# Kernel optimization log

Hardware: AMD Instinct MI355X
Metric: run time of the kernel (lower is better)

The kernel has to match this reference:

```python
import jax, jax.numpy as jnp
import numpy as np

H = 8  # num_heads

def setup_inputs() -> dict:
    key = jax.random.key(0)
    ks = jax.random.split(key, 8)
    N, B, E = 1024, 8, 256
    value = jax.random.normal(ks[0], (N, B, E), dtype=jnp.float32)
    pos = jax.random.normal(ks[1], (B * H, N, N), dtype=jnp.float32)
    s = 1.0 / np.sqrt(E)
    in_proj_w = jax.random.uniform(ks[2], (3 * E, E), jnp.float32, -s, s)   # content attn qkv proj
    in_proj_b = jnp.zeros((3 * E,), jnp.float32)
    out_w = jax.random.uniform(ks[3], (E, E), jnp.float32, -s, s)
    out_b = jnp.zeros((E,), jnp.float32)
    return {"value": value, "position_attention_weights": pos,
            "in_proj_w": in_proj_w, "in_proj_b": in_proj_b,
            "out_w": out_w, "out_b": out_b}

def reference(value, position_attention_weights, in_proj_w, in_proj_b, out_w, out_b):
    # value: (N, B, E) seq-first, position_attention_weights: (B*H, N, N)
    N, B, E = value.shape
    Dh = E // H
    qkv = value @ in_proj_w.T + in_proj_b            # (N, B, 3E)
    q, k, v = jnp.split(qkv, 3, axis=-1)
    # (N, B, E) -> (B*H, N, Dh)
    def to_heads(t):
        return t.reshape(N, B * H, Dh).transpose(1, 0, 2)
    q, k, v = to_heads(q), to_heads(k), to_heads(v)
    scale = 1.0 / jnp.sqrt(jnp.asarray(Dh, q.dtype))
    content = jnp.einsum('bnd,bmd->bnm', q * scale, k)   # (B*H, N, N) content scores
    # merge_attention == 'gate': clamp both, log-sigmoid gate on positional, add
    content = jnp.clip(content, -10.0, 10.0)
    pos = jnp.clip(position_attention_weights, -10.0, 10.0)
    scores = jax.nn.log_sigmoid(pos) + content
    attn = jax.nn.softmax(scores, axis=-1)               # normalizer
    out = jnp.einsum('bnm,bmd->bnd', attn, v)            # (B*H, N, Dh)
    out = out.transpose(1, 0, 2).reshape(N, B, E)        # back to (N, B, E)
    out = out @ out_w.T + out_b
    attn_avg = attn.reshape(B, H, N, N).mean(axis=1)     # averaged attention weights
    return out, attn_avg
```

## Files before the change

kernel.cpp:

```cpp
#include <hip/hip_runtime.h>
#include <hip/hip_bf16.h>

typedef __attribute__((ext_vector_type(8))) short short8;
typedef __attribute__((ext_vector_type(4))) float f32x4;
typedef __attribute__((ext_vector_type(4))) unsigned short u16x4;

#define MFMA16(a,b,c) __builtin_amdgcn_mfma_f32_16x16x32_bf16((a),(b),(c),0,0,0)

__device__ __forceinline__ ushort f2bf(float x) {
  union { float f; unsigned u; } v; v.f = x;
  unsigned u = v.u;
  u = (u + 0x7fffu + ((u >> 16) & 1u)) >> 16;
  return (ushort)u;
}

__device__ __forceinline__ float bf2f(ushort u) {
  union { unsigned u; float f; } v; v.u = ((unsigned)u) << 16;
  return v.f;
}

__device__ __forceinline__ short8 ld8(const ushort* p) {
  return *reinterpret_cast<const short8*>(p);
}

__device__ __forceinline__ f32x4 ld4(const float* p) {
  return *reinterpret_cast<const f32x4*>(p);
}

__global__ void conv_kernel(const float* __restrict__ value,
                            const float* __restrict__ w_in,
                            const float* __restrict__ w_out,
                            ushort* __restrict__ vbf,
                            ushort* __restrict__ wbf,
                            ushort* __restrict__ owbf) {
  int i = blockIdx.x * 256 + threadIdx.x;
  const float* src; ushort* dst; int j;
  if (i < 524288)      { src = value; dst = vbf;  j = i; }
  else if (i < 573440) { src = w_in;  dst = wbf;  j = i - 524288; }
  else                 { src = w_out; dst = owbf; j = i - 573440; }
  float4 v = reinterpret_cast<const float4*>(src)[j];
  u16x4 o;
  o[0] = f2bf(v.x); o[1] = f2bf(v.y); o[2] = f2bf(v.z); o[3] = f2bf(v.w);
  reinterpret_cast<u16x4*>(dst)[j] = o;
}

__global__ __launch_bounds__(256) void qkv_kernel(
    const ushort* __restrict__ vbf, const ushort* __restrict__ wbf,
    const float* __restrict__ bias,
    ushort* __restrict__ qh, ushort* __restrict__ kh, ushort* __restrict__ vv) {
  int tid = threadIdx.x;
  int wave = tid >> 6, lane = tid & 63;
  int lq = lane & 15, lg = lane >> 4;
  int r0 = blockIdx.x * 16;
  int c0 = (blockIdx.y * 4 + wave) * 16;
  f32x4 acc = {0.f, 0.f, 0.f, 0.f};
  const ushort* ap = vbf + (size_t)(r0 + lq) * 256 + lg * 8;
  const ushort* bp = wbf + (size_t)(c0 + lq) * 256 + lg * 8;
#pragma unroll
  for (int k0 = 0; k0 < 256; k0 += 32)
    acc = MFMA16(ld8(ap + k0), ld8(bp + k0), acc);
  int c = c0 + lq;
  float bv = bias[c];
#pragma unroll
  for (int r = 0; r < 4; ++r) {
    int row = r0 + lg * 4 + r;
    int n = row >> 3, b = row & 7;
    float v = acc[r] + bv;
    if (c < 256) {
      int h = c >> 5, d = c & 31;
      qh[((size_t)(b * 8 + h) * 1024 + n) * 32 + d] = f2bf(v * 0.17677669529663689f);
    } else if (c < 512) {
      int cc = c - 256, h = cc >> 5, d = cc & 31;
      kh[((size_t)(b * 8 + h) * 1024 + n) * 32 + d] = f2bf(v);
    } else {
      int cc = c - 512, h = cc >> 5, d = cc & 31;
      vv[((size_t)(b * 8 + h) * 1024 + n) * 32 + d] = f2bf(v);
    }
  }
}

__global__ __launch_bounds__(256) void vtrans_kernel(const ushort* __restrict__ vv,
                                                     ushort* __restrict__ vt) {
  __shared__ ushort t[32][73];
  int tid = threadIdx.x;
  int bh = blockIdx.y, m0 = blockIdx.x * 64;
  int mm = tid >> 2, d0 = (tid & 3) * 8;
  short8 v = ld8(vv + ((size_t)bh * 1024 + m0 + mm) * 32 + d0);
#pragma unroll
  for (int j = 0; j < 8; ++j) t[d0 + j][mm] = (ushort)v[j];
  __syncthreads();
  int d = tid >> 3, mg = (tid & 7) * 8;
  short8 o;
#pragma unroll
  for (int j = 0; j < 8; ++j) o[j] = (short)t[d][mg + j];
  *reinterpret_cast<short8*>(vt + ((size_t)bh * 32 + d) * 1024 + m0 + mg) = o;
}

__global__ __launch_bounds__(256, 2) void attn_kernel(
    const ushort* __restrict__ qh, const ushort* __restrict__ kh,
    const ushort* __restrict__ vt, const float* __restrict__ pos,
    ushort* __restrict__ ao, float* __restrict__ avg_out) {
  __shared__ float pvred[2][4][16][32];
  __shared__ float rowsumT[2][16][4];

  int tid = threadIdx.x;
  int wave = tid >> 6, lane = tid & 63;
  int lq = lane & 15, lg = lane >> 4;
  int b = blockIdx.x;
  int n0 = blockIdx.y * 16;
  int wbase = wave * 256;
  int ra = ((lq >> 2) << 3) + (lq & 3);

  float avg[8][8];
#pragma unroll
  for (int u = 0; u < 8; ++u)
#pragma unroll
    for (int i = 0; i < 8; ++i) avg[u][i] = 0.f;

  const float* pbase = pos + ((size_t)(b * 8) << 20) + (size_t)(n0 + lq) * 1024 + wbase + lg * 8;

  f32x4 pfa[2], pfb[2];
  pfa[0] = ld4(pbase);       pfb[0] = ld4(pbase + 4);
  pfa[1] = ld4(pbase + 32);  pfb[1] = ld4(pbase + 36);

  for (int h = 0; h < 8; ++h) {
    int bh = b * 8 + h;
    const ushort* kp = kh + (size_t)bh * 32768;
    const ushort* vp = vt + (size_t)bh * 32768;
    short8 qa = ld8(qh + ((size_t)bh * 1024 + n0 + lq) * 32 + lg * 8);

    f32x4 acc0 = {0.f, 0.f, 0.f, 0.f}, acc1 = {0.f, 0.f, 0.f, 0.f};
    float rs = 0.f;
    short8 wh[8];

#pragma unroll
    for (int u = 0; u < 8; ++u) {
      int mu = wbase + u * 32;
      f32x4 p0 = pfa[u & 1];
      f32x4 p1 = pfb[u & 1];
      short8 ka = ld8(kp + (size_t)(mu + ra) * 32 + lg * 8);
      short8 kb = ld8(kp + (size_t)(mu + ra + 4) * 32 + lg * 8);
      short8 va = ld8(vp + (size_t)lq * 1024 + mu + lg * 8);
      short8 vb = ld8(vp + (size_t)(lq + 16) * 1024 + mu + lg * 8);
      {
        int g = h * 8 + u + 2;
        int gc = g < 63 ? g : 63;
        const float* np = pbase + ((size_t)(gc >> 3) << 20) + (gc & 7) * 32;
        pfa[u & 1] = ld4(np);
        pfb[u & 1] = ld4(np + 4);
      }
      f32x4 z = {0.f, 0.f, 0.f, 0.f};
      f32x4 SA = MFMA16(ka, qa, z);
      f32x4 SB = MFMA16(kb, qa, z);
      short8 w8;
#pragma unroll
      for (int i = 0; i < 4; ++i) {
        float p = fminf(10.f, fmaxf(-10.f, p0[i]));
        float c = fminf(10.f, fmaxf(-10.f, SA[i]));
        float w = __expf(c - 10.f) * __builtin_amdgcn_rcpf(1.f + __expf(-p));
        rs += w;
        w8[i] = (short)f2bf(w);
      }
#pragma unroll
      for (int i = 0; i < 4; ++i) {
        float p = fminf(10.f, fmaxf(-10.f, p1[i]));
        float c = fminf(10.f, fmaxf(-10.f, SB[i]));
        float w = __expf(c - 10.f) * __builtin_amdgcn_rcpf(1.f + __expf(-p));
        rs += w;
        w8[4 + i] = (short)f2bf(w);
      }
      wh[u] = w8;
      acc0 = MFMA16(w8, va, acc0);
      acc1 = MFMA16(w8, vb, acc1);
    }
    rs += __shfl_xor(rs, 16);
    rs += __shfl_xor(rs, 32);
    int buf = h & 1;
    if (lane < 16) rowsumT[buf][lq][wave] = rs;
#pragma unroll
    for (int j = 0; j < 4; ++j) {
      pvred[buf][wave][lg * 4 + j][lq] = acc0[j];
      pvred[buf][wave][lg * 4 + j][lq + 16] = acc1[j];
    }
    __syncthreads();
    {
      float invr = __builtin_amdgcn_rcpf(rowsumT[buf][lq][0] + rowsumT[buf][lq][1] +
                                         rowsumT[buf][lq][2] + rowsumT[buf][lq][3]);
#pragma unroll
      for (int u = 0; u < 8; ++u)
#pragma unroll
        for (int i = 0; i < 8; ++i)
          avg[u][i] += bf2f((ushort)wh[u][i]) * invr;
      int n = tid >> 4, d = tid & 15;
      float invn = __builtin_amdgcn_rcpf(rowsumT[buf][n][0] + rowsumT[buf][n][1] +
                                         rowsumT[buf][n][2] + rowsumT[buf][n][3]);
      float s0 = pvred[buf][0][n][d] + pvred[buf][1][n][d] +
                 pvred[buf][2][n][d] + pvred[buf][3][n][d];
      float s1 = pvred[buf][0][n][d + 16] + pvred[buf][1][n][d + 16] +
                 pvred[buf][2][n][d + 16] + pvred[buf][3][n][d + 16];
      size_t base = ((size_t)(n0 + n) * 8 + b) * 256 + h * 32;
      ao[base + d] = f2bf(s0 * invn);
      ao[base + d + 16] = f2bf(s1 * invn);
    }
  }
  float* op = avg_out + (size_t)b * 1048576 + (size_t)(n0 + lq) * 1024 + wbase;
#pragma unroll
  for (int u = 0; u < 8; ++u) {
    f32x4 v0 = {avg[u][0] * 0.125f, avg[u][1] * 0.125f, avg[u][2] * 0.125f, avg[u][3] * 0.125f};
    f32x4 v1 = {avg[u][4] * 0.125f, avg[u][5] * 0.125f, avg[u][6] * 0.125f, avg[u][7] * 0.125f};
    __builtin_nontemporal_store(v0, reinterpret_cast<f32x4*>(op + u * 32 + lg * 8));
    __builtin_nontemporal_store(v1, reinterpret_cast<f32x4*>(op + u * 32 + lg * 8 + 4));
  }
}

__global__ __launch_bounds__(256) void oproj_kernel(
    const ushort* __restrict__ ao, const ushort* __restrict__ owbf,
    const float* __restrict__ ob, float* __restrict__ outp) {
  int tid = threadIdx.x;
  int wave = tid >> 6, lane = tid & 63;
  int lq = lane & 15, lg = lane >> 4;
  int r0 = blockIdx.x * 16;
  int c0 = (blockIdx.y * 4 + wave) * 16;
  f32x4 acc = {0.f, 0.f, 0.f, 0.f};
  const ushort* ap = ao + (size_t)(r0 + lq) * 256 + lg * 8;
  const ushort* bp = owbf + (size_t)(c0 + lq) * 256 + lg * 8;
#pragma unroll
  for (int k0 = 0; k0 < 256; k0 += 32)
    acc = MFMA16(ld8(ap + k0), ld8(bp + k0), acc);
  int c = c0 + lq;
  float bv = ob[c];
#pragma unroll
  for (int r = 0; r < 4; ++r) {
    int row = r0 + lg * 4 + r;
    outp[(size_t)row * 256 + c] = acc[r] + bv;
  }
}

extern "C" void kernel_launch(void* const* d_in, const int* in_sizes, int n_in,
                              void* d_out, int out_size, void* d_ws, size_t ws_size,
                              hipStream_t stream) {
  const float* value = (const float*)d_in[0];
  const float* pos   = (const float*)d_in[1];
  const float* w_in  = (const float*)d_in[2];
  const float* b_in  = (const float*)d_in[3];
  const float* w_out = (const float*)d_in[4];
  const float* b_out = (const float*)d_in[5];

  char* ws = (char*)d_ws;
  ushort* vbf  = (ushort*)(ws);
  ushort* wbf  = (ushort*)(ws + 4194304);
  ushort* owbf = (ushort*)(ws + 4587520);
  ushort* qh   = (ushort*)(ws + 4718592);
  ushort* kh   = (ushort*)(ws + 8912896);
  ushort* vv   = (ushort*)(ws + 13107200);
  ushort* vt   = (ushort*)(ws);
  ushort* ao   = (ushort*)(ws + 17301504);

  float* outp = (float*)d_out;
  float* avgp = outp + 2097152;

  conv_kernel<<<2304, 256, 0, stream>>>(value, w_in, w_out, vbf, wbf, owbf);
  qkv_kernel<<<dim3(512, 12), 256, 0, stream>>>(vbf, wbf, b_in, qh, kh, vv);
  vtrans_kernel<<<dim3(16, 64), 256, 0, stream>>>(vv, vt);
  attn_kernel<<<dim3(8, 64), 256, 0, stream>>>(qh, kh, vt, pos, ao, avgp);
  oproj_kernel<<<dim3(512, 4), 256, 0, stream>>>(ao, owbf, b_out, outp);
}
```

Before: 192.2 us.

## Split fused attention into score kernel and PV/average kernel via workspace

```diff
diff --git a/kernel.cpp b/kernel.cpp
--- a/kernel.cpp
+++ b/kernel.cpp
@@ -96,59 +96,33 @@
   *reinterpret_cast<short8*>(vt + ((size_t)bh * 32 + d) * 1024 + m0 + mg) = o;
 }
 
-__global__ __launch_bounds__(256, 2) void attn_kernel(
+__global__ __launch_bounds__(256, 4) void score_kernel(
     const ushort* __restrict__ qh, const ushort* __restrict__ kh,
-    const ushort* __restrict__ vt, const float* __restrict__ pos,
-    ushort* __restrict__ ao, float* __restrict__ avg_out) {
-  __shared__ float pvred[2][4][16][32];
-  __shared__ float rowsumT[2][16][4];
-
+    const float* __restrict__ pos, ushort* __restrict__ wbuf,
+    float* __restrict__ rsum) {
   int tid = threadIdx.x;
   int wave = tid >> 6, lane = tid & 63;
   int lq = lane & 15, lg = lane >> 4;
   int b = blockIdx.x;
   int n0 = blockIdx.y * 16;
-  int wbase = wave * 256;
+  int mh = blockIdx.z;
   int ra = ((lq >> 2) << 3) + (lq & 3);
-
-  float avg[8][8];
-#pragma unroll
-  for (int u = 0; u < 8; ++u)
-#pragma unroll
-    for (int i = 0; i < 8; ++i) avg[u][i] = 0.f;
-
-  const float* pbase = pos + ((size_t)(b * 8) << 20) + (size_t)(n0 + lq) * 1024 + wbase + lg * 8;
-
-  f32x4 pfa[2], pfb[2];
-  pfa[0] = ld4(pbase);       pfb[0] = ld4(pbase + 4);
-  pfa[1] = ld4(pbase + 32);  pfb[1] = ld4(pbase + 36);
+  int mw = mh * 256 + wave * 64;
 
   for (int h = 0; h < 8; ++h) {
     int bh = b * 8 + h;
     const ushort* kp = kh + (size_t)bh * 32768;
-    const ushort* vp = vt + (size_t)bh * 32768;
+    const float* pp = pos + ((size_t)bh << 20) + (size_t)(n0 + lq) * 1024;
+    ushort* wp = wbuf + ((size_t)bh << 20) + (size_t)(n0 + lq) * 1024;
     short8 qa = ld8(qh + ((size_t)bh * 1024 + n0 + lq) * 32 + lg * 8);
-
-    f32x4 acc0 = {0.f, 0.f, 0.f, 0.f}, acc1 = {0.f, 0.f, 0.f, 0.f};
     float rs = 0.f;
-    short8 wh[8];
-
-#pragma unroll
-    for (int u = 0; u < 8; ++u) {
-      int mu = wbase + u * 32;
-      f32x4 p0 = pfa[u & 1];
-      f32x4 p1 = pfb[u & 1];
+#pragma unroll
+    for (int u = 0; u < 2; ++u) {
+      int mu = mw + u * 32;
       short8 ka = ld8(kp + (size_t)(mu + ra) * 32 + lg * 8);
       short8 kb = ld8(kp + (size_t)(mu + ra + 4) * 32 + lg * 8);
-      short8 va = ld8(vp + (size_t)lq * 1024 + mu + lg * 8);
-      short8 vb = ld8(vp + (size_t)(lq + 16) * 1024 + mu + lg * 8);
-      {
-        int g = h * 8 + u + 2;
-        int gc = g < 63 ? g : 63;
-        const float* np = pbase + ((size_t)(gc >> 3) << 20) + (gc & 7) * 32;
-        pfa[u & 1] = ld4(np);
-        pfb[u & 1] = ld4(np + 4);
-      }
+      f32x4 p0 = ld4(pp + mu + lg * 8);
+      f32x4 p1 = ld4(pp + mu + lg * 8 + 4);
       f32x4 z = {0.f, 0.f, 0.f, 0.f};
       f32x4 SA = MFMA16(ka, qa, z);
       f32x4 SB = MFMA16(kb, qa, z);
@@ -169,14 +143,56 @@
         rs += w;
         w8[4 + i] = (short)f2bf(w);
       }
-      wh[u] = w8;
+      *reinterpret_cast<short8*>(wp + mu + lg * 8) = w8;
+    }
+    rs += __shfl_xor(rs, 16);
+    rs += __shfl_xor(rs, 32);
+    if (lane < 16)
+      rsum[(((size_t)bh << 10) + n0 + lq) * 16 + mh * 4 + wave] = rs;
+  }
+}
+
+__global__ __launch_bounds__(256, 3) void pv_kernel(
+    const ushort* __restrict__ wbuf, const float* __restrict__ rsum,
+    const ushort* __restrict__ vt, ushort* __restrict__ ao,
+    float* __restrict__ avg_out) {
+  __shared__ float pvred[2][4][16][32];
+
+  int tid = threadIdx.x;
+  int wave = tid >> 6, lane = tid & 63;
+  int lq = lane & 15, lg = lane >> 4;
+  int b = blockIdx.x;
+  int n0 = blockIdx.y * 16;
+
+  float avg[8][8];
+#pragma unroll
+  for (int u = 0; u < 8; ++u)
+#pragma unroll
+    for (int i = 0; i < 8; ++i) avg[u][i] = 0.f;
+
+  for (int h = 0; h < 8; ++h) {
+    int bh = b * 8 + h;
+    const ushort* vp = vt + (size_t)bh * 32768 + wave * 256 + lg * 8;
+    const ushort* wp = wbuf + ((size_t)bh << 20) + (size_t)(n0 + lq) * 1024 + wave * 256 + lg * 8;
+    const float* rp = rsum + (((size_t)bh << 10) + n0 + lq) * 16;
+    f32x4 s0 = ld4(rp), s1 = ld4(rp + 4), s2 = ld4(rp + 8), s3 = ld4(rp + 12);
+    float invr = __builtin_amdgcn_rcpf(
+        s0[0] + s0[1] + s0[2] + s0[3] + s1[0] + s1[1] + s1[2] + s1[3] +
+        s2[0] + s2[1] + s2[2] + s2[3] + s3[0] + s3[1] + s3[2] + s3[3]);
+
+    f32x4 acc0 = {0.f, 0.f, 0.f, 0.f}, acc1 = {0.f, 0.f, 0.f, 0.f};
+#pragma unroll
+    for (int u = 0; u < 8; ++u) {
+      short8 w8 = ld8(wp + u * 32);
+      short8 va = ld8(vp + (size_t)lq * 1024 + u * 32);
+      short8 vb = ld8(vp + (size_t)(lq + 16) * 1024 + u * 32);
       acc0 = MFMA16(w8, va, acc0);
       acc1 = MFMA16(w8, vb, acc1);
-    }
-    rs += __shfl_xor(rs, 16);
-    rs += __shfl_xor(rs, 32);
+#pragma unroll
+      for (int i = 0; i < 8; ++i)
+        avg[u][i] += bf2f((ushort)w8[i]) * invr;
+    }
     int buf = h & 1;
-    if (lane < 16) rowsumT[buf][lq][wave] = rs;
 #pragma unroll
     for (int j = 0; j < 4; ++j) {
       pvred[buf][wave][lg * 4 + j][lq] = acc0[j];
@@ -184,26 +200,22 @@
     }
     __syncthreads();
     {
-      float invr = __builtin_amdgcn_rcpf(rowsumT[buf][lq][0] + rowsumT[buf][lq][1] +
-                                         rowsumT[buf][lq][2] + rowsumT[buf][lq][3]);
-#pragma unroll
-      for (int u = 0; u < 8; ++u)
-#pragma unroll
-        for (int i = 0; i < 8; ++i)
-          avg[u][i] += bf2f((ushort)wh[u][i]) * invr;
       int n = tid >> 4, d = tid & 15;
-      float invn = __builtin_amdgcn_rcpf(rowsumT[buf][n][0] + rowsumT[buf][n][1] +
-                                         rowsumT[buf][n][2] + rowsumT[buf][n][3]);
-      float s0 = pvred[buf][0][n][d] + pvred[buf][1][n][d] +
+      const float* rp2 = rsum + (((size_t)bh << 10) + n0 + n) * 16;
+      f32x4 t0 = ld4(rp2), t1 = ld4(rp2 + 4), t2 = ld4(rp2 + 8), t3 = ld4(rp2 + 12);
+      float invn = __builtin_amdgcn_rcpf(
+          t0[0] + t0[1] + t0[2] + t0[3] + t1[0] + t1[1] + t1[2] + t1[3] +
+          t2[0] + t2[1] + t2[2] + t2[3] + t3[0] + t3[1] + t3[2] + t3[3]);
+      float v0 = pvred[buf][0][n][d] + pvred[buf][1][n][d] +
                  pvred[buf][2][n][d] + pvred[buf][3][n][d];
-      float s1 = pvred[buf][0][n][d + 16] + pvred[buf][1][n][d + 16] +
+      float v1 = pvred[buf][0][n][d + 16] + pvred[buf][1][n][d + 16] +
                  pvred[buf][2][n][d + 16] + pvred[buf][3][n][d + 16];
       size_t base = ((size_t)(n0 + n) * 8 + b) * 256 + h * 32;
-      ao[base + d] = f2bf(s0 * invn);
-      ao[base + d + 16] = f2bf(s1 * invn);
-    }
-  }
-  float* op = avg_out + (size_t)b * 1048576 + (size_t)(n0 + lq) * 1024 + wbase;
+      ao[base + d] = f2bf(v0 * invn);
+      ao[base + d + 16] = f2bf(v1 * invn);
+    }
+  }
+  float* op = avg_out + (size_t)b * 1048576 + (size_t)(n0 + lq) * 1024 + wave * 256;
 #pragma unroll
   for (int u = 0; u < 8; ++u) {
     f32x4 v0 = {avg[u][0] * 0.125f, avg[u][1] * 0.125f, avg[u][2] * 0.125f, avg[u][3] * 0.125f};
@@ -255,6 +267,8 @@
   ushort* vv   = (ushort*)(ws + 13107200);
   ushort* vt   = (ushort*)(ws);
   ushort* ao   = (ushort*)(ws + 17301504);
+  ushort* wbuf = (ushort*)(ws + 33554432);
+  float*  rsum = (float*)(ws + 167772160);
 
   float* outp = (float*)d_out;
   float* avgp = outp + 2097152;
@@ -262,6 +276,7 @@
   conv_kernel<<<2304, 256, 0, stream>>>(value, w_in, w_out, vbf, wbf, owbf);
   qkv_kernel<<<dim3(512, 12), 256, 0, stream>>>(vbf, wbf, b_in, qh, kh, vv);
   vtrans_kernel<<<dim3(16, 64), 256, 0, stream>>>(vv, vt);
-  attn_kernel<<<dim3(8, 64), 256, 0, stream>>>(qh, kh, vt, pos, ao, avgp);
+  score_kernel<<<dim3(8, 64, 4), 256, 0, stream>>>(qh, kh, pos, wbuf, rsum);
+  pv_kernel<<<dim3(8, 64), 256, 0, stream>>>(wbuf, rsum, vt, ao, avgp);
   oproj_kernel<<<dim3(512, 4), 256, 0, stream>>>(ao, owbf, b_out, outp);
 }
```

Result: slower. 258.0 us (+34.2%).
